# Kernel tuning notes

Measured on AMD Instinct MI355X. Metric: run time of the kernel, lower is better.

## Reference

```python
import jax, jax.numpy as jnp
import numpy as np

EMBED_DIM = 512
NUM_HEADS = 8
TGT_LEN = 2048
SRC_LEN = 2048
BSZ = 4
W_SCALE = 0.02  # keep pre-softmax logits in a sane range


def setup_inputs() -> dict:
    key = jax.random.key(0)
    ks = jax.random.split(key, 13)
    E = EMBED_DIM
    inp = {
        "query": jax.random.normal(ks[0], (TGT_LEN, BSZ, E), jnp.float32),
        "key": jax.random.normal(ks[1], (SRC_LEN, BSZ, E), jnp.float32),
        "value": jax.random.normal(ks[2], (SRC_LEN, BSZ, E), jnp.float32),
        "attn_mask": jax.random.normal(ks[3], (TGT_LEN, SRC_LEN), jnp.float32),
        # Linear params, torch layout: W is [out, in], y = x @ W.T + b
        "Wq": jax.random.normal(ks[4], (E, E), jnp.float32) * W_SCALE,
        "bq": jax.random.normal(ks[5], (E,), jnp.float32) * W_SCALE,
        "Wk": jax.random.normal(ks[6], (E, E), jnp.float32) * W_SCALE,
        "bk": jax.random.normal(ks[7], (E,), jnp.float32) * W_SCALE,
        "Wv": jax.random.normal(ks[8], (E, E), jnp.float32) * W_SCALE,
        "bv": jax.random.normal(ks[9], (E,), jnp.float32) * W_SCALE,
        "Wo": jax.random.normal(ks[10], (E, E), jnp.float32) * W_SCALE,
        "bo": jax.random.normal(ks[11], (E,), jnp.float32) * W_SCALE,
    }
    return inp


def reference(query, key, value, attn_mask, Wq, bq, Wk, bk, Wv, bv, Wo, bo):
    # QAT quant/dequant stubs are identity in float math; dropout p=0 (eval) is identity.
    T, B, E = query.shape
    S = key.shape[0]
    H = NUM_HEADS
    hd = E // H
    scale = hd ** (-0.5)

    q = query @ Wq.T + bq            # [T, B, E]
    k = key @ Wk.T + bk              # [S, B, E]
    v = value @ Wv.T + bv            # [S, B, E]

    q = q.reshape(T, B, H, hd) * scale
    k = k.reshape(S, B, H, hd)
    v = v.reshape(S, B, H, hd)

    # scores: [B, H, T, S]
    scores = jnp.einsum("tbhd,sbhd->bhts", q, k)
    scores = scores + attn_mask[None, None, :, :]  # mask_add.add (float mask)
    attn = jax.nn.softmax(scores, axis=-1)         # SegmentLUTSoftmax == softmax in float

    out = jnp.einsum("bhts,sbhd->tbhd", attn, v).reshape(T, B, E)
    out = out @ Wo.T + bo                          # out_proj

    # need_weights=True, average_attn_weights=True: mean over heads -> [B, T, S]
    attn_weights = jnp.sum(attn, axis=1) * (1.0 / H)
    return out, attn_weights
```

## Files before the change

### kernel.cpp

```cpp
#include <hip/hip_runtime.h>
#include <hip/hip_bf16.h>

#define T_LEN 2048
#define S_LEN 2048
#define BSZ   4
#define EMB   512
#define NHEAD 8
#define HDIM  64

using bf16x8 = __attribute__((ext_vector_type(8))) short;
using f32x4  = __attribute__((ext_vector_type(4))) float;

static __device__ __forceinline__ unsigned short f2bf(float x) {
    __hip_bfloat16 h = __float2bfloat16(x);
    return *reinterpret_cast<unsigned short*>(&h);
}
static __device__ __forceinline__ float bf2f(unsigned short u) {
    __hip_bfloat16 h;
    *reinterpret_cast<unsigned short*>(&h) = u;
    return __bfloat162float(h);
}
static __device__ __forceinline__ unsigned int pk2(float a, float b) {
    return (unsigned)f2bf(a) | ((unsigned)f2bf(b) << 16);
}

__global__ __launch_bounds__(256) void convert_w4(
    const float* __restrict__ W0, const float* __restrict__ W1,
    const float* __restrict__ W2, const float* __restrict__ W3,
    unsigned short* __restrict__ Hi, unsigned short* __restrict__ Lo, int n4)
{
    const int z = blockIdx.y;
    const float* X = (z == 0) ? W0 : (z == 1) ? W1 : (z == 2) ? W2 : W3;
    unsigned short* H = Hi + (size_t)z * (size_t)EMB * EMB;
    unsigned short* L = Lo + (size_t)z * (size_t)EMB * EMB;
    const int stride = gridDim.x * 256;
    for (int i = blockIdx.x * 256 + threadIdx.x; i < n4; i += stride) {
        float4 v = ((const float4*)X)[i];
        unsigned short h0 = f2bf(v.x), h1 = f2bf(v.y), h2 = f2bf(v.z), h3 = f2bf(v.w);
        uint2 ph, pg;
        ph.x = (unsigned)h0 | ((unsigned)h1 << 16);
        ph.y = (unsigned)h2 | ((unsigned)h3 << 16);
        pg.x = pk2(v.x - bf2f(h0), v.y - bf2f(h1));
        pg.y = pk2(v.z - bf2f(h2), v.w - bf2f(h3));
        ((uint2*)H)[i] = ph;
        ((uint2*)L)[i] = pg;
    }
}

template <int MODE, bool XF32>
__global__ __launch_bounds__(256) void proj_mfma(
    const float* __restrict__ Xf,
    const unsigned short* __restrict__ Xhi, const unsigned short* __restrict__ Xlo,
    const unsigned short* __restrict__ Whi, const unsigned short* __restrict__ Wlo,
    const float* __restrict__ bias,
    float* __restrict__ Yf, unsigned short* __restrict__ Yhi, float scale)
{
    const int n0 = blockIdx.x * 64;
    const int m0 = blockIdx.y * 64;

    __shared__ unsigned short whs[64 * 64];
    __shared__ unsigned short wls[64 * 64];
    __shared__ unsigned short xhs[XF32 ? 64 * 64 : 1];
    __shared__ unsigned short xls[XF32 ? 64 * 64 : 1];

    const int tid = threadIdx.x;
    const int w   = tid >> 6;
    const int l   = tid & 63;
    const int l4  = l >> 4, l15 = l & 15;
    const int sw  = (l & 7) << 4;
    char* whsb = (char*)whs;
    char* wlsb = (char*)wls;
    char* xhsb = (char*)xhs;
    char* xlsb = (char*)xls;

    const int srow = tid >> 2;
    const int schk = tid & 3;
    const size_t wbase = (size_t)(n0 + srow) * 512 + schk * 16;
    const int stw = (srow * 128 + schk * 32) ^ ((srow & 7) << 4);

    f32x4 acc[4];
    #pragma unroll
    for (int nb = 0; nb < 4; ++nb) { f32x4 z = {0.f, 0.f, 0.f, 0.f}; acc[nb] = z; }

    uint4 wh0 = *(const uint4*)(Whi + wbase);
    uint4 wh1 = *(const uint4*)(Whi + wbase + 8);
    uint4 wl0 = *(const uint4*)(Wlo + wbase);
    uint4 wl1 = *(const uint4*)(Wlo + wbase + 8);

    const size_t xfbase = (size_t)(m0 + srow) * 512 + schk * 16;
    const size_t xbase  = (size_t)(m0 + w * 16 + l15) * 512 + l4 * 8;
    float4 xp0, xp1, xp2, xp3;
    bf16x8 ah0, ah1, al0, al1;
    if constexpr (XF32) {
        xp0 = *(const float4*)(Xf + xfbase);
        xp1 = *(const float4*)(Xf + xfbase + 4);
        xp2 = *(const float4*)(Xf + xfbase + 8);
        xp3 = *(const float4*)(Xf + xfbase + 12);
    } else {
        ah0 = *(const bf16x8*)(Xhi + xbase);
        ah1 = *(const bf16x8*)(Xhi + xbase + 32);
        al0 = *(const bf16x8*)(Xlo + xbase);
        al1 = *(const bf16x8*)(Xlo + xbase + 32);
    }

    for (int c = 0; c < 8; ++c) {
        __syncthreads();
        *(uint4*)(whsb + stw)        = wh0;
        *(uint4*)(whsb + (stw ^ 16)) = wh1;
        *(uint4*)(wlsb + stw)        = wl0;
        *(uint4*)(wlsb + (stw ^ 16)) = wl1;
        if constexpr (XF32) {
            uint4 H0, H1, L0, L1;
            H0.x = pk2(xp0.x, xp0.y); H0.y = pk2(xp0.z, xp0.w);
            H0.z = pk2(xp1.x, xp1.y); H0.w = pk2(xp1.z, xp1.w);
            H1.x = pk2(xp2.x, xp2.y); H1.y = pk2(xp2.z, xp2.w);
            H1.z = pk2(xp3.x, xp3.y); H1.w = pk2(xp3.z, xp3.w);
            L0.x = pk2(xp0.x - bf2f(f2bf(xp0.x)), xp0.y - bf2f(f2bf(xp0.y)));
            L0.y = pk2(xp0.z - bf2f(f2bf(xp0.z)), xp0.w - bf2f(f2bf(xp0.w)));
            L0.z = pk2(xp1.x - bf2f(f2bf(xp1.x)), xp1.y - bf2f(f2bf(xp1.y)));
            L0.w = pk2(xp1.z - bf2f(f2bf(xp1.z)), xp1.w - bf2f(f2bf(xp1.w)));
            L1.x = pk2(xp2.x - bf2f(f2bf(xp2.x)), xp2.y - bf2f(f2bf(xp2.y)));
            L1.y = pk2(xp2.z - bf2f(f2bf(xp2.z)), xp2.w - bf2f(f2bf(xp2.w)));
            L1.z = pk2(xp3.x - bf2f(f2bf(xp3.x)), xp3.y - bf2f(f2bf(xp3.y)));
            L1.w = pk2(xp3.z - bf2f(f2bf(xp3.z)), xp3.w - bf2f(f2bf(xp3.w)));
            *(uint4*)(xhsb + stw)        = H0;
            *(uint4*)(xhsb + (stw ^ 16)) = H1;
            *(uint4*)(xlsb + stw)        = L0;
            *(uint4*)(xlsb + (stw ^ 16)) = L1;
        }
        __syncthreads();

        bf16x8 cah[2], cal[2];
        if constexpr (XF32) {
            #pragma unroll
            for (int kc = 0; kc < 2; ++kc) {
                const int aoff = (((w * 16 + l15) * 128) + kc * 64 + l4 * 16) ^ sw;
                cah[kc] = *(const bf16x8*)(xhsb + aoff);
                cal[kc] = *(const bf16x8*)(xlsb + aoff);
            }
        } else {
            cah[0] = ah0; cah[1] = ah1; cal[0] = al0; cal[1] = al1;
        }

        if (c < 7) {
            const size_t wb2 = wbase + (size_t)(c + 1) * 64;
            wh0 = *(const uint4*)(Whi + wb2);
            wh1 = *(const uint4*)(Whi + wb2 + 8);
            wl0 = *(const uint4*)(Wlo + wb2);
            wl1 = *(const uint4*)(Wlo + wb2 + 8);
            if constexpr (XF32) {
                const size_t xb2 = xfbase + (size_t)(c + 1) * 64;
                xp0 = *(const float4*)(Xf + xb2);
                xp1 = *(const float4*)(Xf + xb2 + 4);
                xp2 = *(const float4*)(Xf + xb2 + 8);
                xp3 = *(const float4*)(Xf + xb2 + 12);
            } else {
                const size_t xb2 = xbase + (size_t)(c + 1) * 64;
                ah0 = *(const bf16x8*)(Xhi + xb2);
                ah1 = *(const bf16x8*)(Xhi + xb2 + 32);
                al0 = *(const bf16x8*)(Xlo + xb2);
                al1 = *(const bf16x8*)(Xlo + xb2 + 32);
            }
        }

        #pragma unroll
        for (int kc = 0; kc < 2; ++kc) {
            #pragma unroll
            for (int nb = 0; nb < 4; ++nb) {
                const int off = (((nb * 16 + l15) * 128) + kc * 64 + l4 * 16) ^ sw;
                bf16x8 bh = *(const bf16x8*)(whsb + off);
                bf16x8 bl = *(const bf16x8*)(wlsb + off);
                acc[nb] = __builtin_amdgcn_mfma_f32_16x16x32_bf16(cah[kc], bh, acc[nb], 0, 0, 0);
                acc[nb] = __builtin_amdgcn_mfma_f32_16x16x32_bf16(cah[kc], bl, acc[nb], 0, 0, 0);
                acc[nb] = __builtin_amdgcn_mfma_f32_16x16x32_bf16(cal[kc], bh, acc[nb], 0, 0, 0);
            }
        }
    }

    #pragma unroll
    for (int nb = 0; nb < 4; ++nb)
        #pragma unroll
        for (int r = 0; r < 4; ++r) {
            const int m = m0 + w * 16 + l4 * 4 + r;
            const int n = n0 + nb * 16 + l15;
            const float y = (acc[nb][r] + bias[n]) * scale;
            const size_t idx = (size_t)m * 512 + n;
            if constexpr (MODE == 0) Yf[idx] = y;
            else                     Yhi[idx] = f2bf(y);
        }
}

__global__ __launch_bounds__(256) void transpose_v(const unsigned short* __restrict__ V,
                                                   unsigned short* __restrict__ Vt)
{
    const int s0 = blockIdx.x * 64;
    const int h  = blockIdx.y, b = blockIdx.z;
    __shared__ unsigned short tile[64][72];
    const int tid = threadIdx.x;
    {
        const int r = tid >> 2, c = (tid & 3) * 16;
        const unsigned short* src = V + ((size_t)(s0 + r) * BSZ + b) * EMB + h * HDIM + c;
        uint4 u0 = *(const uint4*)(src);
        uint4 u1 = *(const uint4*)(src + 8);
        *(uint4*)&tile[r][c]     = u0;
        *(uint4*)&tile[r][c + 8] = u1;
    }
    __syncthreads();
    {
        const int d = tid >> 2, sg = tid & 3;
        unsigned int w_[8];
        #pragma unroll
        for (int j = 0; j < 8; ++j) {
            unsigned int lo = tile[sg * 16 + 2 * j][d];
            unsigned int hi = tile[sg * 16 + 2 * j + 1][d];
            w_[j] = lo | (hi << 16);
        }
        uint4 o0 = {w_[0], w_[1], w_[2], w_[3]};
        uint4 o1 = {w_[4], w_[5], w_[6], w_[7]};
        unsigned short* dst = Vt + ((size_t)(b * NHEAD + h) * HDIM + d) * S_LEN + s0 + sg * 16;
        *(uint4*)dst       = o0;
        *(uint4*)(dst + 8) = o1;
    }
}

__global__ __launch_bounds__(256) void flash_fwd_mfma(
    const unsigned short* __restrict__ Qbf, const unsigned short* __restrict__ Kbf,
    const unsigned short* __restrict__ Vt,  const float* __restrict__ mask,
    unsigned short* __restrict__ Ohi, unsigned short* __restrict__ Olo,
    float* __restrict__ Lout)
{
    const int tt0 = blockIdx.x * 128;
    const int h   = blockIdx.y, b = blockIdx.z;

    __shared__ unsigned short ks[64 * 64];
    __shared__ unsigned short vs[64 * 64];
    __shared__ unsigned short pl[4][2][16 * 64];

    const int tid = threadIdx.x;
    const int w   = tid >> 6;
    const int l   = tid & 63;
    const int l4  = l >> 4, l15 = l & 15;
    const int sw  = (l & 7) << 4;

    char* ksb = (char*)ks;
    char* vsb = (char*)vs;
    char* pb_[2] = {(char*)pl[w][0], (char*)pl[w][1]};

    bf16x8 qf[2][2];
    #pragma unroll
    for (int a = 0; a < 2; ++a) {
        const int t = tt0 + w * 32 + a * 16 + l15;
        const unsigned short* qp = Qbf + ((size_t)t * BSZ + b) * EMB + h * HDIM + l4 * 8;
        qf[a][0] = *(const bf16x8*)(qp);
        qf[a][1] = *(const bf16x8*)(qp + 32);
    }

    f32x4 oacc[2][4];
    #pragma unroll
    for (int a = 0; a < 2; ++a)
        #pragma unroll
        for (int nb = 0; nb < 4; ++nb) { f32x4 z = {0.f, 0.f, 0.f, 0.f}; oacc[a][nb] = z; }
    float lsum[2] = {0.f, 0.f};

    const int srow = tid >> 2;
    const int schk = tid & 3;
    const unsigned short* kcol = Kbf + (size_t)b * EMB + h * HDIM + schk * 16;
    const unsigned short* vrow = Vt + ((size_t)(b * NHEAD + h) * HDIM + srow) * S_LEN + schk * 16;
    const int stw = (srow * 128 + schk * 32) ^ ((srow & 7) << 4);

    const float* mrowp[2];
    #pragma unroll
    for (int a = 0; a < 2; ++a)
        mrowp[a] = mask + (size_t)(tt0 + w * 32 + a * 16 + l15) * S_LEN + l4 * 4;

    const unsigned short* kp0 = kcol + (size_t)srow * BSZ * EMB;
    uint4 ka0 = *(const uint4*)(kp0);
    uint4 ka1 = *(const uint4*)(kp0 + 8);
    uint4 va0 = *(const uint4*)(vrow);
    uint4 va1 = *(const uint4*)(vrow + 8);

    for (int s0 = 0; s0 < S_LEN; s0 += 64) {
        __syncthreads();
        *(uint4*)(ksb + stw)        = ka0;
        *(uint4*)(ksb + (stw ^ 16)) = ka1;
        *(uint4*)(vsb + stw)        = va0;
        *(uint4*)(vsb + (stw ^ 16)) = va1;
        __syncthreads();

        if (s0 + 64 < S_LEN) {
            const unsigned short* kp2 = kcol + (size_t)(s0 + 64 + srow) * BSZ * EMB;
            ka0 = *(const uint4*)(kp2);
            ka1 = *(const uint4*)(kp2 + 8);
            va0 = *(const uint4*)(vrow + s0 + 64);
            va1 = *(const uint4*)(vrow + s0 + 64 + 8);
        }

        f32x4 sacc[2][4];
        #pragma unroll
        for (int a = 0; a < 2; ++a)
            #pragma unroll
            for (int nb = 0; nb < 4; ++nb) { f32x4 z = {0.f, 0.f, 0.f, 0.f}; sacc[a][nb] = z; }
        #pragma unroll
        for (int kc = 0; kc < 2; ++kc) {
            #pragma unroll
            for (int nb = 0; nb < 4; ++nb) {
                const int off = (((nb * 16 + l15) * 128) + kc * 64 + l4 * 16) ^ sw;
                bf16x8 kf = *(const bf16x8*)(ksb + off);
                sacc[0][nb] = __builtin_amdgcn_mfma_f32_16x16x32_bf16(kf, qf[0][kc], sacc[0][nb], 0, 0, 0);
                sacc[1][nb] = __builtin_amdgcn_mfma_f32_16x16x32_bf16(kf, qf[1][kc], sacc[1][nb], 0, 0, 0);
            }
        }

        #pragma unroll
        for (int a = 0; a < 2; ++a) {
            char* pw = pb_[a];
            #pragma unroll
            for (int nb = 0; nb < 4; ++nb) {
                float4 mk = *(const float4*)(mrowp[a] + s0 + nb * 16);
                const float p0 = __expf(sacc[a][nb][0] + mk.x);
                const float p1 = __expf(sacc[a][nb][1] + mk.y);
                const float p2 = __expf(sacc[a][nb][2] + mk.z);
                const float p3 = __expf(sacc[a][nb][3] + mk.w);
                lsum[a] += (p0 + p1) + (p2 + p3);
                uint2 pk;
                pk.x = pk2(p0, p1);
                pk.y = pk2(p2, p3);
                *(uint2*)(pw + ((l15 * 128 + nb * 32 + l4 * 8) ^ sw)) = pk;
            }
        }

        bf16x8 pa[2][2];
        #pragma unroll
        for (int a = 0; a < 2; ++a) {
            pa[a][0] = *(const bf16x8*)(pb_[a] + ((l15 * 128 + l4 * 16) ^ sw));
            pa[a][1] = *(const bf16x8*)(pb_[a] + ((l15 * 128 + 64 + l4 * 16) ^ sw));
        }
        #pragma unroll
        for (int nb = 0; nb < 4; ++nb) {
            const int off0 = (((nb * 16 + l15) * 128) + l4 * 16) ^ sw;
            bf16x8 vf0 = *(const bf16x8*)(vsb + off0);
            bf16x8 vf1 = *(const bf16x8*)(vsb + (off0 ^ 64));
            oacc[0][nb] = __builtin_amdgcn_mfma_f32_16x16x32_bf16(pa[0][0], vf0, oacc[0][nb], 0, 0, 0);
            oacc[0][nb] = __builtin_amdgcn_mfma_f32_16x16x32_bf16(pa[0][1], vf1, oacc[0][nb], 0, 0, 0);
            oacc[1][nb] = __builtin_amdgcn_mfma_f32_16x16x32_bf16(pa[1][0], vf0, oacc[1][nb], 0, 0, 0);
            oacc[1][nb] = __builtin_amdgcn_mfma_f32_16x16x32_bf16(pa[1][1], vf1, oacc[1][nb], 0, 0, 0);
        }
    }

    #pragma unroll
    for (int a = 0; a < 2; ++a) {
        float lfull = lsum[a];
        lfull += __shfl_xor(lfull, 16);
        lfull += __shfl_xor(lfull, 32);
        float linv[4];
        #pragma unroll
        for (int r = 0; r < 4; ++r)
            linv[r] = 1.0f / __shfl(lfull, l4 * 4 + r);

        #pragma unroll
        for (int nb = 0; nb < 4; ++nb)
            #pragma unroll
            for (int r = 0; r < 4; ++r) {
                const int t = tt0 + w * 32 + a * 16 + l4 * 4 + r;
                const size_t idx = ((size_t)t * BSZ + b) * EMB + h * HDIM + nb * 16 + l15;
                const float y = oacc[a][nb][r] * linv[r];
                const unsigned short hi = f2bf(y);
                Ohi[idx] = hi;
                Olo[idx] = f2bf(y - bf2f(hi));
            }
        if (l < 16)
            Lout[((size_t)b * NHEAD + h) * T_LEN + tt0 + w * 32 + a * 16 + l] = lfull;
    }
}

__global__ __launch_bounds__(256) void attn_weights_mfma(
    const unsigned short* __restrict__ Qhi, const unsigned short* __restrict__ Khi,
    const float* __restrict__ mask, const float* __restrict__ Lin,
    float* __restrict__ Wout)
{
    const int tt0 = blockIdx.x * 128;
    const int ss0 = blockIdx.y * 64;
    const int b   = blockIdx.z;

    __shared__ unsigned short khs[64 * 64];
    __shared__ float lls[NHEAD][128];

    const int tid = threadIdx.x;
    const int w   = tid >> 6;
    const int l   = tid & 63;
    const int l4  = l >> 4, l15 = l & 15;
    const int sw  = (l & 7) << 4;
    char* khsb = (char*)khs;

    for (int i = tid; i < NHEAD * 128; i += 256) {
        const int hh = i >> 7, t2 = i & 127;
        lls[hh][t2] = 1.0f / Lin[(size_t)(b * NHEAD + hh) * T_LEN + tt0 + t2];
    }

    float4 msk[2][4];
    #pragma unroll
    for (int a = 0; a < 2; ++a) {
        const float* mrowp = mask + (size_t)(tt0 + w * 32 + a * 16 + l15) * S_LEN + ss0 + l4 * 4;
        #pragma unroll
        for (int nb = 0; nb < 4; ++nb) msk[a][nb] = *(const float4*)(mrowp + nb * 16);
    }

    float4 wacc[2][4] = {};

    const int srow = tid >> 2;
    const int schk = tid & 3;
    const size_t kbase = ((size_t)(ss0 + srow) * BSZ + b) * EMB + schk * 16;
    const int stw = (srow * 128 + schk * 32) ^ ((srow & 7) << 4);
    size_t qbase[2];
    #pragma unroll
    for (int a = 0; a < 2; ++a)
        qbase[a] = ((size_t)(tt0 + w * 32 + a * 16 + l15) * BSZ + b) * EMB + l4 * 8;

    uint4 kh0 = *(const uint4*)(Khi + kbase);
    uint4 kh1 = *(const uint4*)(Khi + kbase + 8);

    for (int h = 0; h < NHEAD; ++h) {
        __syncthreads();
        *(uint4*)(khsb + stw)        = kh0;
        *(uint4*)(khsb + (stw ^ 16)) = kh1;
        __syncthreads();

        if (h < NHEAD - 1) {
            kh0 = *(const uint4*)(Khi + kbase + (h + 1) * HDIM);
            kh1 = *(const uint4*)(Khi + kbase + (h + 1) * HDIM + 8);
        }

        bf16x8 qh[2][2];
        #pragma unroll
        for (int a = 0; a < 2; ++a) {
            qh[a][0] = *(const bf16x8*)(Qhi + qbase[a] + h * HDIM);
            qh[a][1] = *(const bf16x8*)(Qhi + qbase[a] + h * HDIM + 32);
        }

        f32x4 sacc[2][4];
        #pragma unroll
        for (int a = 0; a < 2; ++a)
            #pragma unroll
            for (int nb = 0; nb < 4; ++nb) { f32x4 z = {0.f, 0.f, 0.f, 0.f}; sacc[a][nb] = z; }
        #pragma unroll
        for (int kc = 0; kc < 2; ++kc) {
            #pragma unroll
            for (int nb = 0; nb < 4; ++nb) {
                const int off = (((nb * 16 + l15) * 128) + kc * 64 + l4 * 16) ^ sw;
                bf16x8 kf = *(const bf16x8*)(khsb + off);
                sacc[0][nb] = __builtin_amdgcn_mfma_f32_16x16x32_bf16(kf, qh[0][kc], sacc[0][nb], 0, 0, 0);
                sacc[1][nb] = __builtin_amdgcn_mfma_f32_16x16x32_bf16(kf, qh[1][kc], sacc[1][nb], 0, 0, 0);
            }
        }

        #pragma unroll
        for (int a = 0; a < 2; ++a) {
            const float lh = lls[h][w * 32 + a * 16 + l15];
            #pragma unroll
            for (int nb = 0; nb < 4; ++nb) {
                wacc[a][nb].x += __expf(sacc[a][nb][0] + msk[a][nb].x) * lh;
                wacc[a][nb].y += __expf(sacc[a][nb][1] + msk[a][nb].y) * lh;
                wacc[a][nb].z += __expf(sacc[a][nb][2] + msk[a][nb].z) * lh;
                wacc[a][nb].w += __expf(sacc[a][nb][3] + msk[a][nb].w) * lh;
            }
        }
    }

    #pragma unroll
    for (int a = 0; a < 2; ++a) {
        float* orow = Wout + ((size_t)b * T_LEN + tt0 + w * 32 + a * 16 + l15) * S_LEN + ss0 + l4 * 4;
        #pragma unroll
        for (int nb = 0; nb < 4; ++nb) {
            float4 o = {wacc[a][nb].x * (1.0f / NHEAD), wacc[a][nb].y * (1.0f / NHEAD),
                        wacc[a][nb].z * (1.0f / NHEAD), wacc[a][nb].w * (1.0f / NHEAD)};
            *(float4*)(orow + nb * 16) = o;
        }
    }
}

extern "C" void kernel_launch(void* const* d_in, const int* in_sizes, int n_in,
                              void* d_out, int out_size, void* d_ws, size_t ws_size,
                              hipStream_t stream)
{
    const float* query = (const float*)d_in[0];
    const float* key   = (const float*)d_in[1];
    const float* value = (const float*)d_in[2];
    const float* mask  = (const float*)d_in[3];
    const float* Wq    = (const float*)d_in[4];
    const float* bq    = (const float*)d_in[5];
    const float* Wk    = (const float*)d_in[6];
    const float* bk    = (const float*)d_in[7];
    const float* Wv    = (const float*)d_in[8];
    const float* bv    = (const float*)d_in[9];
    const float* Wo    = (const float*)d_in[10];
    const float* bo    = (const float*)d_in[11];

    float* out = (float*)d_out;

    const size_t NQKV = (size_t)T_LEN * BSZ * EMB;
    const size_t NW   = (size_t)EMB * EMB;

    unsigned short* qhi = (unsigned short*)d_ws;
    unsigned short* khi = qhi + NQKV;
    unsigned short* vhi = khi + NQKV;
    unsigned short* whb = vhi + NQKV;
    unsigned short* wlb = whb + 4 * NW;
    float* lb = (float*)(wlb + 4 * NW);

    unsigned short* wqh = whb + 0 * NW, *wql = wlb + 0 * NW;
    unsigned short* wkh = whb + 1 * NW, *wkl = wlb + 1 * NW;
    unsigned short* wvh = whb + 2 * NW, *wvl = wlb + 2 * NW;
    unsigned short* woh = whb + 3 * NW, *wol = wlb + 3 * NW;

    unsigned short* vt  = (unsigned short*)(out + NQKV);
    unsigned short* cxh = (unsigned short*)(out + NQKV + 3000000);
    unsigned short* cxl = (unsigned short*)(out + NQKV + 6000000);

    const dim3 gproj(8, 128);

    convert_w4<<<dim3(64, 4), 256, 0, stream>>>(Wq, Wk, Wv, Wo, whb, wlb, (int)(NW / 4));

    proj_mfma<2, true><<<gproj, 256, 0, stream>>>(query, nullptr, nullptr, wqh, wql, bq,
                                                  nullptr, qhi, 0.125f);
    proj_mfma<2, true><<<gproj, 256, 0, stream>>>(key, nullptr, nullptr, wkh, wkl, bk,
                                                  nullptr, khi, 1.0f);
    proj_mfma<2, true><<<gproj, 256, 0, stream>>>(value, nullptr, nullptr, wvh, wvl, bv,
                                                  nullptr, vhi, 1.0f);

    transpose_v<<<dim3(S_LEN / 64, NHEAD, BSZ), 256, 0, stream>>>(vhi, vt);

    flash_fwd_mfma<<<dim3(T_LEN / 128, NHEAD, BSZ), 256, 0, stream>>>(
        qhi, khi, vt, mask, cxh, cxl, lb);

    proj_mfma<0, false><<<gproj, 256, 0, stream>>>(nullptr, cxh, cxl, woh, wol, bo,
                                                   out, nullptr, 1.0f);

    attn_weights_mfma<<<dim3(T_LEN / 128, S_LEN / 64, BSZ), 256, 0, stream>>>(
        qhi, khi, mask, lb, out + NQKV);
}
```

Baseline: 257.7 us.

## Drop split-bf16 in QKV projections and double-buffer K/V tiles in attention

Adds a SPLIT template flag so the Q/K/V projections use a single bf16 MFMA per tile instead of the three-term hi/lo compensated product, which removes the low-part loads, conversions and two thirds of the MFMAs. Only the output projection keeps the split. Separately, the flash-attention and attention-weights kernels now double-buffer their K/V shared-memory tiles, cutting one barrier per iteration and overlapping the next tile's stores with compute. The precision drop in Q/K/V raises numerical error, and the extra shared memory may lower occupancy.

```diff
diff --git a/kernel.cpp b/kernel.cpp
--- a/kernel.cpp
+++ b/kernel.cpp
@@ -47,7 +47,7 @@
     }
 }
 
-template <int MODE, bool XF32>
+template <int MODE, bool XF32, bool SPLIT>
 __global__ __launch_bounds__(256) void proj_mfma(
     const float* __restrict__ Xf,
     const unsigned short* __restrict__ Xhi, const unsigned short* __restrict__ Xlo,
@@ -59,9 +59,9 @@
     const int m0 = blockIdx.y * 64;
 
     __shared__ unsigned short whs[64 * 64];
-    __shared__ unsigned short wls[64 * 64];
+    __shared__ unsigned short wls[SPLIT ? 64 * 64 : 1];
     __shared__ unsigned short xhs[XF32 ? 64 * 64 : 1];
-    __shared__ unsigned short xls[XF32 ? 64 * 64 : 1];
+    __shared__ unsigned short xls[(XF32 && SPLIT) ? 64 * 64 : 1];
 
     const int tid = threadIdx.x;
     const int w   = tid >> 6;
@@ -84,8 +84,11 @@
 
     uint4 wh0 = *(const uint4*)(Whi + wbase);
     uint4 wh1 = *(const uint4*)(Whi + wbase + 8);
-    uint4 wl0 = *(const uint4*)(Wlo + wbase);
-    uint4 wl1 = *(const uint4*)(Wlo + wbase + 8);
+    uint4 wl0, wl1;
+    if constexpr (SPLIT) {
+        wl0 = *(const uint4*)(Wlo + wbase);
+        wl1 = *(const uint4*)(Wlo + wbase + 8);
+    }
 
     const size_t xfbase = (size_t)(m0 + srow) * 512 + schk * 16;
     const size_t xbase  = (size_t)(m0 + w * 16 + l15) * 512 + l4 * 8;
@@ -99,34 +102,41 @@
     } else {
         ah0 = *(const bf16x8*)(Xhi + xbase);
         ah1 = *(const bf16x8*)(Xhi + xbase + 32);
-        al0 = *(const bf16x8*)(Xlo + xbase);
-        al1 = *(const bf16x8*)(Xlo + xbase + 32);
+        if constexpr (SPLIT) {
+            al0 = *(const bf16x8*)(Xlo + xbase);
+            al1 = *(const bf16x8*)(Xlo + xbase + 32);
+        }
     }
 
     for (int c = 0; c < 8; ++c) {
         __syncthreads();
         *(uint4*)(whsb + stw)        = wh0;
         *(uint4*)(whsb + (stw ^ 16)) = wh1;
-        *(uint4*)(wlsb + stw)        = wl0;
-        *(uint4*)(wlsb + (stw ^ 16)) = wl1;
+        if constexpr (SPLIT) {
+            *(uint4*)(wlsb + stw)        = wl0;
+            *(uint4*)(wlsb + (stw ^ 16)) = wl1;
+        }
         if constexpr (XF32) {
-            uint4 H0, H1, L0, L1;
+            uint4 H0, H1;
             H0.x = pk2(xp0.x, xp0.y); H0.y = pk2(xp0.z, xp0.w);
             H0.z = pk2(xp1.x, xp1.y); H0.w = pk2(xp1.z, xp1.w);
             H1.x = pk2(xp2.x, xp2.y); H1.y = pk2(xp2.z, xp2.w);
             H1.z = pk2(xp3.x, xp3.y); H1.w = pk2(xp3.z, xp3.w);
-            L0.x = pk2(xp0.x - bf2f(f2bf(xp0.x)), xp0.y - bf2f(f2bf(xp0.y)));
-            L0.y = pk2(xp0.z - bf2f(f2bf(xp0.z)), xp0.w - bf2f(f2bf(xp0.w)));
-            L0.z = pk2(xp1.x - bf2f(f2bf(xp1.x)), xp1.y - bf2f(f2bf(xp1.y)));
-            L0.w = pk2(xp1.z - bf2f(f2bf(xp1.z)), xp1.w - bf2f(f2bf(xp1.w)));
-            L1.x = pk2(xp2.x - bf2f(f2bf(xp2.x)), xp2.y - bf2f(f2bf(xp2.y)));
-            L1.y = pk2(xp2.z - bf2f(f2bf(xp2.z)), xp2.w - bf2f(f2bf(xp2.w)));
-            L1.z = pk2(xp3.x - bf2f(f2bf(xp3.x)), xp3.y - bf2f(f2bf(xp3.y)));
-            L1.w = pk2(xp3.z - bf2f(f2bf(xp3.z)), xp3.w - bf2f(f2bf(xp3.w)));
             *(uint4*)(xhsb + stw)        = H0;
             *(uint4*)(xhsb + (stw ^ 16)) = H1;
-            *(uint4*)(xlsb + stw)        = L0;
-            *(uint4*)(xlsb + (stw ^ 16)) = L1;
+            if constexpr (SPLIT) {
+                uint4 L0, L1;
+                L0.x = pk2(xp0.x - bf2f(f2bf(xp0.x)), xp0.y - bf2f(f2bf(xp0.y)));
+                L0.y = pk2(xp0.z - bf2f(f2bf(xp0.z)), xp0.w - bf2f(f2bf(xp0.w)));
+                L0.z = pk2(xp1.x - bf2f(f2bf(xp1.x)), xp1.y - bf2f(f2bf(xp1.y)));
+                L0.w = pk2(xp1.z - bf2f(f2bf(xp1.z)), xp1.w - bf2f(f2bf(xp1.w)));
+                L1.x = pk2(xp2.x - bf2f(f2bf(xp2.x)), xp2.y - bf2f(f2bf(xp2.y)));
+                L1.y = pk2(xp2.z - bf2f(f2bf(xp2.z)), xp2.w - bf2f(f2bf(xp2.w)));
+                L1.z = pk2(xp3.x - bf2f(f2bf(xp3.x)), xp3.y - bf2f(f2bf(xp3.y)));
+                L1.w = pk2(xp3.z - bf2f(f2bf(xp3.z)), xp3.w - bf2f(f2bf(xp3.w)));
+                *(uint4*)(xlsb + stw)        = L0;
+                *(uint4*)(xlsb + (stw ^ 16)) = L1;
+            }
         }
         __syncthreads();
 
@@ -136,18 +146,21 @@
             for (int kc = 0; kc < 2; ++kc) {
                 const int aoff = (((w * 16 + l15) * 128) + kc * 64 + l4 * 16) ^ sw;
                 cah[kc] = *(const bf16x8*)(xhsb + aoff);
-                cal[kc] = *(const bf16x8*)(xlsb + aoff);
+                if constexpr (SPLIT) cal[kc] = *(const bf16x8*)(xlsb + aoff);
             }
         } else {
-            cah[0] = ah0; cah[1] = ah1; cal[0] = al0; cal[1] = al1;
+            cah[0] = ah0; cah[1] = ah1;
+            if constexpr (SPLIT) { cal[0] = al0; cal[1] = al1; }
         }
 
         if (c < 7) {
             const size_t wb2 = wbase + (size_t)(c + 1) * 64;
             wh0 = *(const uint4*)(Whi + wb2);
             wh1 = *(const uint4*)(Whi + wb2 + 8);
-            wl0 = *(const uint4*)(Wlo + wb2);
-            wl1 = *(const uint4*)(Wlo + wb2 + 8);
+            if constexpr (SPLIT) {
+                wl0 = *(const uint4*)(Wlo + wb2);
+                wl1 = *(const uint4*)(Wlo + wb2 + 8);
+            }
             if constexpr (XF32) {
                 const size_t xb2 = xfbase + (size_t)(c + 1) * 64;
                 xp0 = *(const float4*)(Xf + xb2);
@@ -158,8 +171,10 @@
                 const size_t xb2 = xbase + (size_t)(c + 1) * 64;
                 ah0 = *(const bf16x8*)(Xhi + xb2);
                 ah1 = *(const bf16x8*)(Xhi + xb2 + 32);
-                al0 = *(const bf16x8*)(Xlo + xb2);
-                al1 = *(const bf16x8*)(Xlo + xb2 + 32);
+                if constexpr (SPLIT) {
+                    al0 = *(const bf16x8*)(Xlo + xb2);
+                    al1 = *(const bf16x8*)(Xlo + xb2 + 32);
+                }
             }
         }
 
@@ -169,10 +184,12 @@
             for (int nb = 0; nb < 4; ++nb) {
                 const int off = (((nb * 16 + l15) * 128) + kc * 64 + l4 * 16) ^ sw;
                 bf16x8 bh = *(const bf16x8*)(whsb + off);
-                bf16x8 bl = *(const bf16x8*)(wlsb + off);
                 acc[nb] = __builtin_amdgcn_mfma_f32_16x16x32_bf16(cah[kc], bh, acc[nb], 0, 0, 0);
-                acc[nb] = __builtin_amdgcn_mfma_f32_16x16x32_bf16(cah[kc], bl, acc[nb], 0, 0, 0);
-                acc[nb] = __builtin_amdgcn_mfma_f32_16x16x32_bf16(cal[kc], bh, acc[nb], 0, 0, 0);
+                if constexpr (SPLIT) {
+                    bf16x8 bl = *(const bf16x8*)(wlsb + off);
+                    acc[nb] = __builtin_amdgcn_mfma_f32_16x16x32_bf16(cah[kc], bl, acc[nb], 0, 0, 0);
+                    acc[nb] = __builtin_amdgcn_mfma_f32_16x16x32_bf16(cal[kc], bh, acc[nb], 0, 0, 0);
+                }
             }
         }
     }
@@ -232,8 +249,8 @@
     const int tt0 = blockIdx.x * 128;
     const int h   = blockIdx.y, b = blockIdx.z;
 
-    __shared__ unsigned short ks[64 * 64];
-    __shared__ unsigned short vs[64 * 64];
+    __shared__ unsigned short ks[2][64 * 64];
+    __shared__ unsigned short vs[2][64 * 64];
     __shared__ unsigned short pl[4][2][16 * 64];
 
     const int tid = threadIdx.x;
@@ -242,8 +259,6 @@
     const int l4  = l >> 4, l15 = l & 15;
     const int sw  = (l & 7) << 4;
 
-    char* ksb = (char*)ks;
-    char* vsb = (char*)vs;
     char* pb_[2] = {(char*)pl[w][0], (char*)pl[w][1]};
 
     bf16x8 qf[2][2];
@@ -273,21 +288,32 @@
     for (int a = 0; a < 2; ++a)
         mrowp[a] = mask + (size_t)(tt0 + w * 32 + a * 16 + l15) * S_LEN + l4 * 4;
 
-    const unsigned short* kp0 = kcol + (size_t)srow * BSZ * EMB;
-    uint4 ka0 = *(const uint4*)(kp0);
-    uint4 ka1 = *(const uint4*)(kp0 + 8);
-    uint4 va0 = *(const uint4*)(vrow);
-    uint4 va1 = *(const uint4*)(vrow + 8);
-
-    for (int s0 = 0; s0 < S_LEN; s0 += 64) {
-        __syncthreads();
-        *(uint4*)(ksb + stw)        = ka0;
-        *(uint4*)(ksb + (stw ^ 16)) = ka1;
-        *(uint4*)(vsb + stw)        = va0;
-        *(uint4*)(vsb + (stw ^ 16)) = va1;
-        __syncthreads();
-
-        if (s0 + 64 < S_LEN) {
+    {
+        const unsigned short* kp0 = kcol + (size_t)srow * BSZ * EMB;
+        uint4 a0 = *(const uint4*)(kp0);
+        uint4 a1 = *(const uint4*)(kp0 + 8);
+        uint4 b0 = *(const uint4*)(vrow);
+        uint4 b1 = *(const uint4*)(vrow + 8);
+        char* k0 = (char*)ks[0];
+        char* v0 = (char*)vs[0];
+        *(uint4*)(k0 + stw)        = a0;
+        *(uint4*)(k0 + (stw ^ 16)) = a1;
+        *(uint4*)(v0 + stw)        = b0;
+        *(uint4*)(v0 + (stw ^ 16)) = b1;
+    }
+    __syncthreads();
+
+    uint4 ka0, ka1, va0, va1;
+    const int NT = S_LEN / 64;
+
+    for (int it = 0; it < NT; ++it) {
+        const int s0  = it * 64;
+        const int cur = it & 1;
+        char* ksb = (char*)ks[cur];
+        char* vsb = (char*)vs[cur];
+        const bool haveNext = (it + 1 < NT);
+
+        if (haveNext) {
             const unsigned short* kp2 = kcol + (size_t)(s0 + 64 + srow) * BSZ * EMB;
             ka0 = *(const uint4*)(kp2);
             ka1 = *(const uint4*)(kp2 + 8);
@@ -345,6 +371,16 @@
             oacc[1][nb] = __builtin_amdgcn_mfma_f32_16x16x32_bf16(pa[1][0], vf0, oacc[1][nb], 0, 0, 0);
             oacc[1][nb] = __builtin_amdgcn_mfma_f32_16x16x32_bf16(pa[1][1], vf1, oacc[1][nb], 0, 0, 0);
         }
+
+        if (haveNext) {
+            char* kn = (char*)ks[cur ^ 1];
+            char* vn = (char*)vs[cur ^ 1];
+            *(uint4*)(kn + stw)        = ka0;
+            *(uint4*)(kn + (stw ^ 16)) = ka1;
+            *(uint4*)(vn + stw)        = va0;
+            *(uint4*)(vn + (stw ^ 16)) = va1;
+        }
+        __syncthreads();
     }
 
     #pragma unroll
@@ -382,7 +418,7 @@
     const int ss0 = blockIdx.y * 64;
     const int b   = blockIdx.z;
 
-    __shared__ unsigned short khs[64 * 64];
+    __shared__ unsigned short khs[2][64 * 64];
     __shared__ float lls[NHEAD][128];
 
     const int tid = threadIdx.x;
@@ -390,7 +426,6 @@
     const int l   = tid & 63;
     const int l4  = l >> 4, l15 = l & 15;
     const int sw  = (l & 7) << 4;
-    char* khsb = (char*)khs;
 
     for (int i = tid; i < NHEAD * 128; i += 256) {
         const int hh = i >> 7, t2 = i & 127;
@@ -416,16 +451,23 @@
     for (int a = 0; a < 2; ++a)
         qbase[a] = ((size_t)(tt0 + w * 32 + a * 16 + l15) * BSZ + b) * EMB + l4 * 8;
 
-    uint4 kh0 = *(const uint4*)(Khi + kbase);
-    uint4 kh1 = *(const uint4*)(Khi + kbase + 8);
+    {
+        uint4 a0 = *(const uint4*)(Khi + kbase);
+        uint4 a1 = *(const uint4*)(Khi + kbase + 8);
+        char* k0 = (char*)khs[0];
+        *(uint4*)(k0 + stw)        = a0;
+        *(uint4*)(k0 + (stw ^ 16)) = a1;
+    }
+    __syncthreads();
+
+    uint4 kh0, kh1;
 
     for (int h = 0; h < NHEAD; ++h) {
-        __syncthreads();
-        *(uint4*)(khsb + stw)        = kh0;
-        *(uint4*)(khsb + (stw ^ 16)) = kh1;
-        __syncthreads();
-
-        if (h < NHEAD - 1) {
+        const int cur = h & 1;
+        char* khsb = (char*)khs[cur];
+        const bool haveNext = (h + 1 < NHEAD);
+
+        if (haveNext) {
             kh0 = *(const uint4*)(Khi + kbase + (h + 1) * HDIM);
             kh1 = *(const uint4*)(Khi + kbase + (h + 1) * HDIM + 8);
         }
@@ -464,6 +506,13 @@
                 wacc[a][nb].w += __expf(sacc[a][nb][3] + msk[a][nb].w) * lh;
             }
         }
+
+        if (haveNext) {
+            char* kn = (char*)khs[cur ^ 1];
+            *(uint4*)(kn + stw)        = kh0;
+            *(uint4*)(kn + (stw ^ 16)) = kh1;
+        }
+        __syncthreads();
     }
 
     #pragma unroll
@@ -507,9 +556,9 @@
     unsigned short* wlb = whb + 4 * NW;
     float* lb = (float*)(wlb + 4 * NW);
 
-    unsigned short* wqh = whb + 0 * NW, *wql = wlb + 0 * NW;
-    unsigned short* wkh = whb + 1 * NW, *wkl = wlb + 1 * NW;
-    unsigned short* wvh = whb + 2 * NW, *wvl = wlb + 2 * NW;
+    unsigned short* wqh = whb + 0 * NW;
+    unsigned short* wkh = whb + 1 * NW;
+    unsigned short* wvh = whb + 2 * NW;
     unsigned short* woh = whb + 3 * NW, *wol = wlb + 3 * NW;
 
     unsigned short* vt  = (unsigned short*)(out + NQKV);
@@ -520,20 +569,20 @@
 
     convert_w4<<<dim3(64, 4), 256, 0, stream>>>(Wq, Wk, Wv, Wo, whb, wlb, (int)(NW / 4));
 
-    proj_mfma<2, true><<<gproj, 256, 0, stream>>>(query, nullptr, nullptr, wqh, wql, bq,
-                                                  nullptr, qhi, 0.125f);
-    proj_mfma<2, true><<<gproj, 256, 0, stream>>>(key, nullptr, nullptr, wkh, wkl, bk,
-                                                  nullptr, khi, 1.0f);
-    proj_mfma<2, true><<<gproj, 256, 0, stream>>>(value, nullptr, nullptr, wvh, wvl, bv,
-                                                  nullptr, vhi, 1.0f);
+    proj_mfma<2, true, false><<<gproj, 256, 0, stream>>>(query, nullptr, nullptr, wqh, nullptr,
+                                                         bq, nullptr, qhi, 0.125f);
+    proj_mfma<2, true, false><<<gproj, 256, 0, stream>>>(key, nullptr, nullptr, wkh, nullptr,
+                                                         bk, nullptr, khi, 1.0f);
+    proj_mfma<2, true, false><<<gproj, 256, 0, stream>>>(value, nullptr, nullptr, wvh, nullptr,
+                                                         bv, nullptr, vhi, 1.0f);
 
     transpose_v<<<dim3(S_LEN / 64, NHEAD, BSZ), 256, 0, stream>>>(vhi, vt);
 
     flash_fwd_mfma<<<dim3(T_LEN / 128, NHEAD, BSZ), 256, 0, stream>>>(
         qhi, khi, vt, mask, cxh, cxl, lb);
 
-    proj_mfma<0, false><<<gproj, 256, 0, stream>>>(nullptr, cxh, cxl, woh, wol, bo,
-                                                   out, nullptr, 1.0f);
+    proj_mfma<0, false, true><<<gproj, 256, 0, stream>>>(nullptr, cxh, cxl, woh, wol, bo,
+                                                         out, nullptr, 1.0f);
 
     attn_weights_mfma<<<dim3(T_LEN / 128, S_LEN / 64, BSZ), 256, 0, stream>>>(
         qhi, khi, mask, lb, out + NQKV);
```

Measured after the change: 274.3 us. 6.5% more time.
